# Optimization experiments

Measured on AMD Instinct MI355X. Metric: run time of the kernel, lower is better.

Reference implementation:

```python
import jax, jax.numpy as jnp
import numpy as np

FEATURE_DIM = 512
D_ENERGY = 64


def setup_inputs() -> dict:
    key = jax.random.key(0)
    k1, k2, k3, k4, k5 = jax.random.split(key, 5)
    B, S = 4, 4096
    features = jax.random.normal(k1, (B, S, FEATURE_DIM), dtype=jnp.float32)
    # nn.Linear(feature_dim, d_energy, bias=False) weights, stored as [in, out]
    Wq = jax.random.normal(k2, (FEATURE_DIM, D_ENERGY), dtype=jnp.float32) / np.sqrt(FEATURE_DIM)
    Wk = jax.random.normal(k3, (FEATURE_DIM, D_ENERGY), dtype=jnp.float32) / np.sqrt(FEATURE_DIM)
    # charge_proj: Linear(feature_dim, 1, bias=True)
    w_charge = jax.random.normal(k4, (FEATURE_DIM,), dtype=jnp.float32) / np.sqrt(FEATURE_DIM)
    b_charge = jax.random.normal(k5, (), dtype=jnp.float32)
    locality_scale = jnp.float32(1.0)
    return {"features": features, "Wq": Wq, "Wk": Wk,
            "w_charge": w_charge, "b_charge": b_charge,
            "locality_scale": locality_scale}


def reference(features, Wq, Wk, w_charge, b_charge, locality_scale):
    B, S, F = features.shape
    # compatibility: QK^T / sqrt(d_energy)
    Q = jnp.einsum('bsf,fd->bsd', features, Wq)
    K = jnp.einsum('bsf,fd->bsd', features, Wk)
    scores = jnp.einsum('bid,bjd->bij', Q, K) / jnp.sqrt(jnp.float32(D_ENERGY))
    # locality bias: locality_scale / clamp(|i-j|, 1)
    pos = jnp.arange(S, dtype=jnp.float32)
    dist = jnp.maximum(jnp.abs(pos[None, :] - pos[:, None]), 1.0)  # [S,S]
    scores = scores * (locality_scale / dist)
    # charge gating: sigmoid(charge_proj(features))
    charge = jax.nn.sigmoid(jnp.einsum('bsf,f->bs', features, w_charge) + b_charge)  # [B,S]
    # energy: -scores * charge_i * charge_j
    energy = -scores * charge[:, :, None] * charge[:, None, :]
    return energy
```

## Files before the change

kernel.cpp:

```cpp
#include <hip/hip_runtime.h>
#include <stdint.h>

#define S 4096
#define BB 4
#define F 512
#define D 64
#define NROW (BB * S)

typedef float f32x4 __attribute__((ext_vector_type(4)));
typedef short s16x8 __attribute__((ext_vector_type(8)));

__device__ __forceinline__ unsigned short f2bf(float f) {
    union { float f; uint32_t u; } v; v.f = f;
    uint32_t u = v.u;
    return (unsigned short)((u + 0x7FFFu + ((u >> 16) & 1u)) >> 16);
}
__device__ __forceinline__ float bf2f(unsigned short h) {
    union { float f; uint32_t u; } v; v.u = ((uint32_t)h) << 16;
    return v.f;
}

__global__ __launch_bounds__(256) void k_split(
        const float* __restrict__ feat, const float* __restrict__ wc,
        const float* __restrict__ bc,
        unsigned short* __restrict__ fH, unsigned short* __restrict__ fL,
        float* __restrict__ charge) {
    int wave = threadIdx.x >> 6, lane = threadIdx.x & 63;
    int row = blockIdx.x * 4 + wave;
    const float* fr = feat + (size_t)row * F + lane * 8;
    f32x4 a = *(const f32x4*)fr;
    f32x4 b = *(const f32x4*)(fr + 4);
    const float* wr = wc + lane * 8;
    f32x4 wa = *(const f32x4*)wr;
    f32x4 wb = *(const f32x4*)(wr + 4);
    float p = a.x*wa.x + a.y*wa.y + a.z*wa.z + a.w*wa.w
            + b.x*wb.x + b.y*wb.y + b.z*wb.z + b.w*wb.w;
    #pragma unroll
    for (int o = 32; o; o >>= 1) p += __shfl_xor(p, o);

    float vals[8] = {a.x, a.y, a.z, a.w, b.x, b.y, b.z, b.w};
    unsigned short h[8], l[8];
    #pragma unroll
    for (int m = 0; m < 8; m++) {
        h[m] = f2bf(vals[m]);
        l[m] = f2bf(vals[m] - bf2f(h[m]));
    }
    *(uint4*)(fH + (size_t)row * F + lane * 8) = *(const uint4*)h;
    *(uint4*)(fL + (size_t)row * F + lane * 8) = *(const uint4*)l;
    if (lane == 0) charge[row] = 1.f / (1.f + expf(-(p + bc[0])));
}

__global__ __launch_bounds__(256) void k_wt(
        const float* __restrict__ Wq, const float* __restrict__ Wk,
        unsigned short* __restrict__ wtH, unsigned short* __restrict__ wtL) {
    int t = blockIdx.x * 256 + threadIdx.x;
    int c = t >> 7;
    int k0 = (t & 127) * 4;
    const float* src = (c < 64) ? (Wq + c) : (Wk + (c - 64));
    unsigned short h[4], l[4];
    #pragma unroll
    for (int j = 0; j < 4; j++) {
        float v = src[(size_t)(k0 + j) * D];
        h[j] = f2bf(v);
        l[j] = f2bf(v - bf2f(h[j]));
    }
    *(uint2*)(wtH + (size_t)c * F + k0) = *(const uint2*)h;
    *(uint2*)(wtL + (size_t)c * F + k0) = *(const uint2*)l;
}

__global__ __launch_bounds__(256) void k_qk(
        const unsigned short* __restrict__ fH, const unsigned short* __restrict__ fL,
        const unsigned short* __restrict__ wtH, const unsigned short* __restrict__ wtL,
        const float* __restrict__ charge, const float* __restrict__ lsp,
        unsigned short* __restrict__ qH, unsigned short* __restrict__ qL,
        unsigned short* __restrict__ kH, unsigned short* __restrict__ kL) {
    int wave = threadIdx.x >> 6, lane = threadIdx.x & 63;
    int col = lane & 15, kg = lane >> 4;
    int row0 = blockIdx.x * 64 + wave * 16;

    f32x4 acc[8];
    #pragma unroll
    for (int j = 0; j < 8; j++) acc[j] = (f32x4)0.f;

    size_t aoff = (size_t)(row0 + col) * F + kg * 8;
    for (int ks = 0; ks < 16; ks++) {
        s16x8 ah = *(const s16x8*)(fH + aoff + ks * 32);
        s16x8 al = *(const s16x8*)(fL + aoff + ks * 32);
        #pragma unroll
        for (int ju = 0; ju < 8; ju++) {
            size_t boff = (size_t)(ju * 16 + col) * F + ks * 32 + kg * 8;
            s16x8 bh = *(const s16x8*)(wtH + boff);
            s16x8 bl = *(const s16x8*)(wtL + boff);
            acc[ju] = __builtin_amdgcn_mfma_f32_16x16x32_bf16(ah, bh, acc[ju], 0, 0, 0);
            acc[ju] = __builtin_amdgcn_mfma_f32_16x16x32_bf16(ah, bl, acc[ju], 0, 0, 0);
            acc[ju] = __builtin_amdgcn_mfma_f32_16x16x32_bf16(al, bh, acc[ju], 0, 0, 0);
        }
    }

    float ls = lsp[0];
    #pragma unroll
    for (int ju = 0; ju < 8; ju++) {
        int c = ju * 16 + col;
        #pragma unroll
        for (int r = 0; r < 4; r++) {
            int row = row0 + kg * 4 + r;
            float ch = charge[row];
            float v = acc[ju][r];
            float sc;
            unsigned short *dh, *dl;
            if (c < 64) { sc = -0.125f * ls * ch; dh = qH; dl = qL; }
            else        { sc = ch;               dh = kH; dl = kL; }
            int cc = c & 63;
            float q = v * sc;
            unsigned short hh = f2bf(q);
            unsigned short ll = f2bf(q - bf2f(hh));
            dh[(size_t)row * D + cc] = hh;
            dl[(size_t)row * D + cc] = ll;
        }
    }
}

__global__ __launch_bounds__(256) void k_energy(
        const unsigned short* __restrict__ qH, const unsigned short* __restrict__ qL,
        const unsigned short* __restrict__ kH, const unsigned short* __restrict__ kL,
        float* __restrict__ out) {
    int wave = threadIdx.x >> 6, lane = threadIdx.x & 63;
    int col = lane & 15, kg = lane >> 4;
    int jt = blockIdx.x, it = blockIdx.y, b = blockIdx.z;
    int i0 = it * 128 + wave * 32;
    int j0 = jt * 64;
    size_t base = (size_t)b * S;

    s16x8 qfh[2][2], qfl[2][2];
    #pragma unroll
    for (int iu = 0; iu < 2; iu++) {
        size_t ro = (base + i0 + iu * 16 + col) * D + kg * 8;
        #pragma unroll
        for (int kh2 = 0; kh2 < 2; kh2++) {
            qfh[iu][kh2] = *(const s16x8*)(qH + ro + kh2 * 32);
            qfl[iu][kh2] = *(const s16x8*)(qL + ro + kh2 * 32);
        }
    }

    f32x4 acc[2][4];
    #pragma unroll
    for (int iu = 0; iu < 2; iu++)
        #pragma unroll
        for (int ju = 0; ju < 4; ju++) acc[iu][ju] = (f32x4)0.f;

    #pragma unroll
    for (int ju = 0; ju < 4; ju++) {
        size_t ro = (base + j0 + ju * 16 + col) * D + kg * 8;
        s16x8 kf0 = *(const s16x8*)(kH + ro);
        s16x8 kf1 = *(const s16x8*)(kH + ro + 32);
        s16x8 kg0 = *(const s16x8*)(kL + ro);
        s16x8 kg1 = *(const s16x8*)(kL + ro + 32);
        #pragma unroll
        for (int iu = 0; iu < 2; iu++) {
            f32x4 a = acc[iu][ju];
            a = __builtin_amdgcn_mfma_f32_16x16x32_bf16(qfh[iu][0], kf0, a, 0, 0, 0);
            a = __builtin_amdgcn_mfma_f32_16x16x32_bf16(qfh[iu][1], kf1, a, 0, 0, 0);
            a = __builtin_amdgcn_mfma_f32_16x16x32_bf16(qfh[iu][0], kg0, a, 0, 0, 0);
            a = __builtin_amdgcn_mfma_f32_16x16x32_bf16(qfh[iu][1], kg1, a, 0, 0, 0);
            a = __builtin_amdgcn_mfma_f32_16x16x32_bf16(qfl[iu][0], kf0, a, 0, 0, 0);
            a = __builtin_amdgcn_mfma_f32_16x16x32_bf16(qfl[iu][1], kf1, a, 0, 0, 0);
            acc[iu][ju] = a;
        }
    }

    #pragma unroll
    for (int iu = 0; iu < 2; iu++)
        #pragma unroll
        for (int ju = 0; ju < 4; ju++)
            #pragma unroll
            for (int r = 0; r < 4; r++) {
                int i = i0 + iu * 16 + kg * 4 + r;
                int j = j0 + ju * 16 + col;
                float dist = fmaxf(fabsf((float)(i - j)), 1.0f);
                out[(base + i) * (size_t)S + j] =
                    acc[iu][ju][r] * __builtin_amdgcn_rcpf(dist);
            }
}

extern "C" void kernel_launch(void* const* d_in, const int* in_sizes, int n_in,
                              void* d_out, int out_size, void* d_ws, size_t ws_size,
                              hipStream_t stream) {
    const float* feat = (const float*)d_in[0];
    const float* Wq   = (const float*)d_in[1];
    const float* Wk   = (const float*)d_in[2];
    const float* wc   = (const float*)d_in[3];
    const float* bc   = (const float*)d_in[4];
    const float* ls   = (const float*)d_in[5];
    float* out = (float*)d_out;

    char* ws = (char*)d_ws;
    unsigned short* fH  = (unsigned short*)ws;                 ws += (size_t)NROW * F * 2;
    unsigned short* fL  = (unsigned short*)ws;                 ws += (size_t)NROW * F * 2;
    unsigned short* wtH = (unsigned short*)ws;                 ws += (size_t)128 * F * 2;
    unsigned short* wtL = (unsigned short*)ws;                 ws += (size_t)128 * F * 2;
    float*          chg = (float*)ws;                          ws += (size_t)NROW * 4;
    unsigned short* qH  = (unsigned short*)ws;                 ws += (size_t)NROW * D * 2;
    unsigned short* qL  = (unsigned short*)ws;                 ws += (size_t)NROW * D * 2;
    unsigned short* kH  = (unsigned short*)ws;                 ws += (size_t)NROW * D * 2;
    unsigned short* kL  = (unsigned short*)ws;                 ws += (size_t)NROW * D * 2;

    hipLaunchKernelGGL(k_split, dim3(NROW / 4), dim3(256), 0, stream,
                       feat, wc, bc, fH, fL, chg);
    hipLaunchKernelGGL(k_wt, dim3(64), dim3(256), 0, stream, Wq, Wk, wtH, wtL);
    hipLaunchKernelGGL(k_qk, dim3(NROW / 64), dim3(256), 0, stream,
                       fH, fL, wtH, wtL, chg, ls, qH, qL, kH, kL);
    hipLaunchKernelGGL(k_energy, dim3(S / 64, S / 128, BB), dim3(256), 0, stream,
                       qH, qL, kH, kL, out);
}
```

Before: 398.0 us.

## Fuse feature split and charge into QK projection; vectorize energy stores

Removes the separate k_split kernel. The QK projection now reads fp32 features directly, splits them into bf16 hi/lo in registers and computes the charge dot product and sigmoid in the same pass, so the 32MB hi/lo feature intermediates are never written or read back. The projection grid changes to 16 rows per block, with each wave covering 32 output columns. The energy kernel swaps MFMA operands so each lane holds 4 consecutive j values and can issue 16-byte vector stores, and its j tile doubles to 128. In exchange, feature rows are read redundantly by all four waves of a block, and the larger energy tile uses more accumulator registers.

```diff
diff --git a/kernel.cpp b/kernel.cpp
--- a/kernel.cpp
+++ b/kernel.cpp
@@ -18,36 +18,6 @@
 __device__ __forceinline__ float bf2f(unsigned short h) {
     union { float f; uint32_t u; } v; v.u = ((uint32_t)h) << 16;
     return v.f;
-}
-
-__global__ __launch_bounds__(256) void k_split(
-        const float* __restrict__ feat, const float* __restrict__ wc,
-        const float* __restrict__ bc,
-        unsigned short* __restrict__ fH, unsigned short* __restrict__ fL,
-        float* __restrict__ charge) {
-    int wave = threadIdx.x >> 6, lane = threadIdx.x & 63;
-    int row = blockIdx.x * 4 + wave;
-    const float* fr = feat + (size_t)row * F + lane * 8;
-    f32x4 a = *(const f32x4*)fr;
-    f32x4 b = *(const f32x4*)(fr + 4);
-    const float* wr = wc + lane * 8;
-    f32x4 wa = *(const f32x4*)wr;
-    f32x4 wb = *(const f32x4*)(wr + 4);
-    float p = a.x*wa.x + a.y*wa.y + a.z*wa.z + a.w*wa.w
-            + b.x*wb.x + b.y*wb.y + b.z*wb.z + b.w*wb.w;
-    #pragma unroll
-    for (int o = 32; o; o >>= 1) p += __shfl_xor(p, o);
-
-    float vals[8] = {a.x, a.y, a.z, a.w, b.x, b.y, b.z, b.w};
-    unsigned short h[8], l[8];
-    #pragma unroll
-    for (int m = 0; m < 8; m++) {
-        h[m] = f2bf(vals[m]);
-        l[m] = f2bf(vals[m] - bf2f(h[m]));
-    }
-    *(uint4*)(fH + (size_t)row * F + lane * 8) = *(const uint4*)h;
-    *(uint4*)(fL + (size_t)row * F + lane * 8) = *(const uint4*)l;
-    if (lane == 0) charge[row] = 1.f / (1.f + expf(-(p + bc[0])));
 }
 
 __global__ __launch_bounds__(256) void k_wt(
@@ -68,27 +38,44 @@
     *(uint2*)(wtL + (size_t)c * F + k0) = *(const uint2*)l;
 }
 
-__global__ __launch_bounds__(256) void k_qk(
-        const unsigned short* __restrict__ fH, const unsigned short* __restrict__ fL,
+__global__ __launch_bounds__(256) void k_qk2(
+        const float* __restrict__ feat,
         const unsigned short* __restrict__ wtH, const unsigned short* __restrict__ wtL,
-        const float* __restrict__ charge, const float* __restrict__ lsp,
+        const float* __restrict__ wc, const float* __restrict__ bc,
+        const float* __restrict__ lsp,
         unsigned short* __restrict__ qH, unsigned short* __restrict__ qL,
         unsigned short* __restrict__ kH, unsigned short* __restrict__ kL) {
     int wave = threadIdx.x >> 6, lane = threadIdx.x & 63;
     int col = lane & 15, kg = lane >> 4;
-    int row0 = blockIdx.x * 64 + wave * 16;
-
-    f32x4 acc[8];
-    #pragma unroll
-    for (int j = 0; j < 8; j++) acc[j] = (f32x4)0.f;
-
-    size_t aoff = (size_t)(row0 + col) * F + kg * 8;
+    int row0 = blockIdx.x * 16;
+    int c0 = wave * 32;
+
+    f32x4 acc[2];
+    acc[0] = (f32x4)0.f; acc[1] = (f32x4)0.f;
+    float psum = 0.f;
+
+    const float* arow = feat + (size_t)(row0 + col) * F + kg * 8;
+    #pragma unroll 4
     for (int ks = 0; ks < 16; ks++) {
-        s16x8 ah = *(const s16x8*)(fH + aoff + ks * 32);
-        s16x8 al = *(const s16x8*)(fL + aoff + ks * 32);
-        #pragma unroll
-        for (int ju = 0; ju < 8; ju++) {
-            size_t boff = (size_t)(ju * 16 + col) * F + ks * 32 + kg * 8;
+        f32x4 a0 = *(const f32x4*)(arow + ks * 32);
+        f32x4 a1 = *(const f32x4*)(arow + ks * 32 + 4);
+        const float* wr = wc + ks * 32 + kg * 8;
+        f32x4 w0 = *(const f32x4*)wr;
+        f32x4 w1 = *(const f32x4*)(wr + 4);
+        psum += a0.x*w0.x + a0.y*w0.y + a0.z*w0.z + a0.w*w0.w
+              + a1.x*w1.x + a1.y*w1.y + a1.z*w1.z + a1.w*w1.w;
+
+        float vals[8] = {a0.x, a0.y, a0.z, a0.w, a1.x, a1.y, a1.z, a1.w};
+        s16x8 ah, al;
+        #pragma unroll
+        for (int m = 0; m < 8; m++) {
+            unsigned short hh = f2bf(vals[m]);
+            ah[m] = (short)hh;
+            al[m] = (short)f2bf(vals[m] - bf2f(hh));
+        }
+        #pragma unroll
+        for (int ju = 0; ju < 2; ju++) {
+            size_t boff = (size_t)(c0 + ju * 16 + col) * F + ks * 32 + kg * 8;
             s16x8 bh = *(const s16x8*)(wtH + boff);
             s16x8 bl = *(const s16x8*)(wtL + boff);
             acc[ju] = __builtin_amdgcn_mfma_f32_16x16x32_bf16(ah, bh, acc[ju], 0, 0, 0);
@@ -97,25 +84,28 @@
         }
     }
 
+    psum += __shfl_xor(psum, 16);
+    psum += __shfl_xor(psum, 32);
+    float sig = 1.f / (1.f + expf(-(psum + bc[0])));
     float ls = lsp[0];
-    #pragma unroll
-    for (int ju = 0; ju < 8; ju++) {
-        int c = ju * 16 + col;
+
+    bool isQ = (c0 < 64);
+    unsigned short* __restrict__ dh = isQ ? qH : kH;
+    unsigned short* __restrict__ dl = isQ ? qL : kL;
+    int ccb = (c0 & 63) + col;
+    #pragma unroll
+    for (int ju = 0; ju < 2; ju++) {
         #pragma unroll
         for (int r = 0; r < 4; r++) {
-            int row = row0 + kg * 4 + r;
-            float ch = charge[row];
-            float v = acc[ju][r];
-            float sc;
-            unsigned short *dh, *dl;
-            if (c < 64) { sc = -0.125f * ls * ch; dh = qH; dl = qL; }
-            else        { sc = ch;               dh = kH; dl = kL; }
-            int cc = c & 63;
-            float q = v * sc;
-            unsigned short hh = f2bf(q);
-            unsigned short ll = f2bf(q - bf2f(hh));
-            dh[(size_t)row * D + cc] = hh;
-            dl[(size_t)row * D + cc] = ll;
+            int rl = kg * 4 + r;
+            float ch = __shfl(sig, rl);
+            float sc = isQ ? (-0.125f * ls * ch) : ch;
+            float v = acc[ju][r] * sc;
+            unsigned short hh = f2bf(v);
+            unsigned short ll = f2bf(v - bf2f(hh));
+            size_t off = (size_t)(row0 + rl) * D + ccb + ju * 16;
+            dh[off] = hh;
+            dl[off] = ll;
         }
     }
 }
@@ -127,59 +117,62 @@
     int wave = threadIdx.x >> 6, lane = threadIdx.x & 63;
     int col = lane & 15, kg = lane >> 4;
     int jt = blockIdx.x, it = blockIdx.y, b = blockIdx.z;
-    int i0 = it * 128 + wave * 32;
-    int j0 = jt * 64;
+    int i0w = it * 128 + wave * 32;
+    int j0 = jt * 128;
     size_t base = (size_t)b * S;
 
-    s16x8 qfh[2][2], qfl[2][2];
+    s16x8 qbh[2][2], qbl[2][2];
     #pragma unroll
     for (int iu = 0; iu < 2; iu++) {
-        size_t ro = (base + i0 + iu * 16 + col) * D + kg * 8;
+        size_t ro = (base + i0w + iu * 16 + col) * (size_t)D + kg * 8;
         #pragma unroll
         for (int kh2 = 0; kh2 < 2; kh2++) {
-            qfh[iu][kh2] = *(const s16x8*)(qH + ro + kh2 * 32);
-            qfl[iu][kh2] = *(const s16x8*)(qL + ro + kh2 * 32);
-        }
-    }
-
-    f32x4 acc[2][4];
+            qbh[iu][kh2] = *(const s16x8*)(qH + ro + kh2 * 32);
+            qbl[iu][kh2] = *(const s16x8*)(qL + ro + kh2 * 32);
+        }
+    }
+
+    f32x4 acc[2][8];
     #pragma unroll
     for (int iu = 0; iu < 2; iu++)
         #pragma unroll
-        for (int ju = 0; ju < 4; ju++) acc[iu][ju] = (f32x4)0.f;
-
-    #pragma unroll
-    for (int ju = 0; ju < 4; ju++) {
-        size_t ro = (base + j0 + ju * 16 + col) * D + kg * 8;
+        for (int ju = 0; ju < 8; ju++) acc[iu][ju] = (f32x4)0.f;
+
+    #pragma unroll
+    for (int ju = 0; ju < 8; ju++) {
+        size_t ro = (base + j0 + ju * 16 + col) * (size_t)D + kg * 8;
         s16x8 kf0 = *(const s16x8*)(kH + ro);
         s16x8 kf1 = *(const s16x8*)(kH + ro + 32);
-        s16x8 kg0 = *(const s16x8*)(kL + ro);
-        s16x8 kg1 = *(const s16x8*)(kL + ro + 32);
+        s16x8 kl0 = *(const s16x8*)(kL + ro);
+        s16x8 kl1 = *(const s16x8*)(kL + ro + 32);
         #pragma unroll
         for (int iu = 0; iu < 2; iu++) {
             f32x4 a = acc[iu][ju];
-            a = __builtin_amdgcn_mfma_f32_16x16x32_bf16(qfh[iu][0], kf0, a, 0, 0, 0);
-            a = __builtin_amdgcn_mfma_f32_16x16x32_bf16(qfh[iu][1], kf1, a, 0, 0, 0);
-            a = __builtin_amdgcn_mfma_f32_16x16x32_bf16(qfh[iu][0], kg0, a, 0, 0, 0);
-            a = __builtin_amdgcn_mfma_f32_16x16x32_bf16(qfh[iu][1], kg1, a, 0, 0, 0);
-            a = __builtin_amdgcn_mfma_f32_16x16x32_bf16(qfl[iu][0], kf0, a, 0, 0, 0);
-            a = __builtin_amdgcn_mfma_f32_16x16x32_bf16(qfl[iu][1], kf1, a, 0, 0, 0);
+            a = __builtin_amdgcn_mfma_f32_16x16x32_bf16(kf0, qbh[iu][0], a, 0, 0, 0);
+            a = __builtin_amdgcn_mfma_f32_16x16x32_bf16(kf1, qbh[iu][1], a, 0, 0, 0);
+            a = __builtin_amdgcn_mfma_f32_16x16x32_bf16(kf0, qbl[iu][0], a, 0, 0, 0);
+            a = __builtin_amdgcn_mfma_f32_16x16x32_bf16(kf1, qbl[iu][1], a, 0, 0, 0);
+            a = __builtin_amdgcn_mfma_f32_16x16x32_bf16(kl0, qbh[iu][0], a, 0, 0, 0);
+            a = __builtin_amdgcn_mfma_f32_16x16x32_bf16(kl1, qbh[iu][1], a, 0, 0, 0);
             acc[iu][ju] = a;
         }
     }
 
     #pragma unroll
-    for (int iu = 0; iu < 2; iu++)
-        #pragma unroll
-        for (int ju = 0; ju < 4; ju++)
-            #pragma unroll
-            for (int r = 0; r < 4; r++) {
-                int i = i0 + iu * 16 + kg * 4 + r;
-                int j = j0 + ju * 16 + col;
-                float dist = fmaxf(fabsf((float)(i - j)), 1.0f);
-                out[(base + i) * (size_t)S + j] =
-                    acc[iu][ju][r] * __builtin_amdgcn_rcpf(dist);
-            }
+    for (int iu = 0; iu < 2; iu++) {
+        int i = i0w + iu * 16 + col;
+        #pragma unroll
+        for (int ju = 0; ju < 8; ju++) {
+            int jb = j0 + ju * 16 + kg * 4;
+            float di = (float)(i - jb);
+            f32x4 v = acc[iu][ju];
+            v.x *= __builtin_amdgcn_rcpf(fmaxf(fabsf(di), 1.0f));
+            v.y *= __builtin_amdgcn_rcpf(fmaxf(fabsf(di - 1.0f), 1.0f));
+            v.z *= __builtin_amdgcn_rcpf(fmaxf(fabsf(di - 2.0f), 1.0f));
+            v.w *= __builtin_amdgcn_rcpf(fmaxf(fabsf(di - 3.0f), 1.0f));
+            *(f32x4*)(out + (base + i) * (size_t)S + jb) = v;
+        }
+    }
 }
 
 extern "C" void kernel_launch(void* const* d_in, const int* in_sizes, int n_in,
@@ -194,21 +187,16 @@
     float* out = (float*)d_out;
 
     char* ws = (char*)d_ws;
-    unsigned short* fH  = (unsigned short*)ws;                 ws += (size_t)NROW * F * 2;
-    unsigned short* fL  = (unsigned short*)ws;                 ws += (size_t)NROW * F * 2;
-    unsigned short* wtH = (unsigned short*)ws;                 ws += (size_t)128 * F * 2;
-    unsigned short* wtL = (unsigned short*)ws;                 ws += (size_t)128 * F * 2;
-    float*          chg = (float*)ws;                          ws += (size_t)NROW * 4;
-    unsigned short* qH  = (unsigned short*)ws;                 ws += (size_t)NROW * D * 2;
-    unsigned short* qL  = (unsigned short*)ws;                 ws += (size_t)NROW * D * 2;
-    unsigned short* kH  = (unsigned short*)ws;                 ws += (size_t)NROW * D * 2;
-    unsigned short* kL  = (unsigned short*)ws;                 ws += (size_t)NROW * D * 2;
-
-    hipLaunchKernelGGL(k_split, dim3(NROW / 4), dim3(256), 0, stream,
-                       feat, wc, bc, fH, fL, chg);
+    unsigned short* wtH = (unsigned short*)ws;  ws += (size_t)128 * F * 2;
+    unsigned short* wtL = (unsigned short*)ws;  ws += (size_t)128 * F * 2;
+    unsigned short* qH  = (unsigned short*)ws;  ws += (size_t)NROW * D * 2;
+    unsigned short* qL  = (unsigned short*)ws;  ws += (size_t)NROW * D * 2;
+    unsigned short* kH  = (unsigned short*)ws;  ws += (size_t)NROW * D * 2;
+    unsigned short* kL  = (unsigned short*)ws;  ws += (size_t)NROW * D * 2;
+
     hipLaunchKernelGGL(k_wt, dim3(64), dim3(256), 0, stream, Wq, Wk, wtH, wtL);
-    hipLaunchKernelGGL(k_qk, dim3(NROW / 64), dim3(256), 0, stream,
-                       fH, fL, wtH, wtL, chg, ls, qH, qL, kH, kL);
-    hipLaunchKernelGGL(k_energy, dim3(S / 64, S / 128, BB), dim3(256), 0, stream,
+    hipLaunchKernelGGL(k_qk2, dim3(NROW / 16), dim3(256), 0, stream,
+                       feat, wtH, wtL, wc, bc, ls, qH, qL, kH, kL);
+    hipLaunchKernelGGL(k_energy, dim3(S / 128, S / 128, BB), dim3(256), 0, stream,
                        qH, qL, kH, kL, out);
 }
```

Result: no change. 393.5 us (-1.2%).
